# Kernel optimization log

Hardware: AMD Instinct MI355X
Metric: run time of the kernel (lower is better)

## Reference

```python
import jax, jax.numpy as jnp
import numpy as np

FS = 2048
LOWER_FREQ = 16.0
UPPER_FREQ = 512.0
N_SCALES = 64
SIZE_FACTOR = 1.0


def _build_ricker_bank():
    # Geometric scale grid from 1/upper_freq to 1/lower_freq
    s0 = 1.0 / UPPER_FREQ
    sn = 1.0 / LOWER_FREQ
    base = np.power(sn / s0, 1.0 / (N_SCALES - 1))
    scales = s0 * np.power(base, np.arange(N_SCALES))  # [n_scales]
    truncation = scales.max() * np.sqrt(4.5) * FS
    one_side = int(SIZE_FACTOR * truncation)
    kernel_size = 2 * one_side + 1  # 543 for these settings
    k = np.arange(kernel_size, dtype=np.float32) - one_side
    t = k / FS  # [K]
    s = scales[:, None].astype(np.float32)  # [n_scales, 1]
    A = 2.0 / (np.sqrt(3.0 * s) * np.pi ** 0.25)
    scaled_t = t[None, :] / s
    bank = A * (1.0 - scaled_t ** 2) * np.exp(-t[None, :] ** 2 / (2.0 * s ** 2))
    return jnp.asarray(bank, dtype=jnp.float32)  # [n_scales, K]


def setup_inputs() -> dict:
    key = jax.random.key(0)
    inputs = jax.random.normal(key, (128, 4096), dtype=jnp.float32)
    W = _build_ricker_bank()  # [64, 543]
    return {"inputs": inputs, "W": W}


def reference(inputs, W):
    # inputs: [B, T]; W: [n_scales, K] Ricker wavelet bank (real-only).
    # Torch does conv2d on [B,1,T,1] with weight [n_scales,1,K,1], padding K//2
    # (K odd -> 'same' length). border_crop=0, imaginary_part=None, so the
    # scalogram is just the real convolution output.
    K = W.shape[1]
    out = jax.lax.conv_general_dilated(
        inputs[:, None, :],          # [B, 1, T]
        W[:, None, :],               # [n_scales, 1, K]
        window_strides=(1,),
        padding=[(K // 2, K // 2)],
        dimension_numbers=("NCH", "OIH", "NCH"),
    )
    return out  # [B, n_scales, T]
```

## Files before the change

### kernel.cpp

```cpp
#include <hip/hip_runtime.h>


#define TLEN  4096
#define NSC   64
#define KLEN  543
#define KPAD  544
#define PADL  271
#define BLOCK 256
#define TT    512
#define XSRC  1056
#define XLEN  1048
#define XREG  1048
#define NKS   34

typedef __attribute__((ext_vector_type(8)))  short  short8;
typedef __attribute__((ext_vector_type(16))) float  float16v;
typedef __attribute__((ext_vector_type(4)))  float  float4v;

__device__ __forceinline__ ushort f2bf(float f) {
    unsigned u = __builtin_bit_cast(unsigned, f);
    unsigned r = (u + 0x7FFFu + ((u >> 16) & 1u)) >> 16;
    return (ushort)r;
}

__global__ __launch_bounds__(256)
void wconv(const float* __restrict__ W, ushort* __restrict__ wpk)
{
    int idx  = blockIdx.x * 256 + threadIdx.x;
    int e    = idx & 7;
    int lane = (idx >> 3) & 63;
    int st   = (idx >> 9) & 1;
    int ks   = idx >> 10;
    int n    = lane & 31;
    int q5   = lane >> 5;
    int s    = 32 * st + n;
    int k    = 16 * ks + 8 * q5 + e;
    float v  = (k < KLEN) ? W[(size_t)s * KLEN + k] : 0.0f;
    wpk[idx] = f2bf(v);
}

__global__ __launch_bounds__(BLOCK, 2)
void ricker_mfma2(const float* __restrict__ x,
                  const ushort* __restrict__ wpk,
                  float* __restrict__ out)
{
    __shared__ __align__(16) ushort xraw[XSRC];
    __shared__ __align__(16) ushort xsm[8 * XREG];

    const int tid    = threadIdx.x;
    const int tTile  = blockIdx.x;
    const int b      = blockIdx.y;
    const int tStart = tTile * TT;

    const float* xrow = x + (size_t)b * TLEN;
    for (int i = tid; i < XSRC; i += BLOCK) {
        int g = tStart - PADL + i;
        float v = (g >= 0 && g < TLEN) ? xrow[g] : 0.0f;
        xraw[i] = f2bf(v);
    }
    __syncthreads();

    for (int idx = tid; idx < 8 * XLEN; idx += BLOCK) {
        int c = idx / XLEN;
        int i = idx - c * XLEN;
        xsm[c * XREG + i] = xraw[i + c];
    }
    __syncthreads();

    const int lane = tid & 63;
    const int wv   = tid >> 6;
    const int n    = lane & 31;
    const int q5   = lane >> 5;
    const int wt0  = wv * 128;

    const ushort* abase = &xsm[(n & 7) * XREG + 8 * (n >> 3) + 8 * q5 + wt0];
    const ushort* bbase = wpk + (size_t)lane * 8;

    float16v acc[4][2];
    #pragma unroll
    for (int tt = 0; tt < 4; ++tt)
        #pragma unroll
        for (int st = 0; st < 2; ++st)
            #pragma unroll
            for (int e = 0; e < 16; ++e) acc[tt][st][e] = 0.f;

    #pragma unroll 2
    for (int ks = 0; ks < NKS; ++ks) {
        const int K0 = 16 * ks;
        const int BO = 1024 * ks;
        short8 bb0 = *(const short8*)&bbase[BO];
        short8 bb1 = *(const short8*)&bbase[BO + 512];
        short8 a[4];
        #pragma unroll
        for (int tt = 0; tt < 4; ++tt)
            a[tt] = *(const short8*)&abase[K0 + 32 * tt];
        #pragma unroll
        for (int tt = 0; tt < 4; ++tt) {
            acc[tt][0] = __builtin_amdgcn_mfma_f32_32x32x16_bf16(a[tt], bb0, acc[tt][0], 0, 0, 0);
            acc[tt][1] = __builtin_amdgcn_mfma_f32_32x32x16_bf16(a[tt], bb1, acc[tt][1], 0, 0, 0);
        }
    }

    const int tb = tStart + wt0 + 4 * q5;
    float* obase = out + (size_t)b * NSC * TLEN;
    #pragma unroll
    for (int st = 0; st < 2; ++st) {
        #pragma unroll
        for (int tt = 0; tt < 4; ++tt) {
            float16v A = acc[tt][st];
            float* o = obase + (size_t)(32 * st + n) * TLEN + tb + 32 * tt;
            #pragma unroll
            for (int r4 = 0; r4 < 4; ++r4) {
                *(float4v*)&o[8 * r4] =
                    (float4v){A[4 * r4], A[4 * r4 + 1], A[4 * r4 + 2], A[4 * r4 + 3]};
            }
        }
    }
}

extern "C" void kernel_launch(void* const* d_in, const int* in_sizes, int n_in,
                              void* d_out, int out_size, void* d_ws, size_t ws_size,
                              hipStream_t stream) {
    const float* x   = (const float*)d_in[0];
    const float* W   = (const float*)d_in[1];
    float*       out = (float*)d_out;
    ushort*      wpk = (ushort*)d_ws;

    wconv<<<dim3((NSC * KPAD) / 256), dim3(256), 0, stream>>>(W, wpk);
    dim3 grid(TLEN / TT, 128);
    ricker_mfma2<<<grid, dim3(BLOCK), 0, stream>>>(x, wpk, out);
}
```

Measured before the change: 165.1 us.

## Stream weight tiles into LDS with async global_load_lds multi-stage pipeline

Replaces direct per-iteration global loads of the packed weight fragments with a 4-deep per-wave ring buffer filled by global_load_lds, using explicit vmcnt waits so the loads for upcoming k-steps overlap the MFMA work. The MFMA block is wrapped in s_setprio to favour matrix issue. The shifted-copy construction of the input tile is also vectorised to 16-byte short8 reads and writes. This adds 32KB of LDS per block, which may lower occupancy below the two blocks per CU requested in launch bounds. The hand-written waitcnt values also have to match the compiler's emitted loads exactly.

```diff
diff --git a/kernel.cpp b/kernel.cpp
--- a/kernel.cpp
+++ b/kernel.cpp
@@ -46,6 +46,7 @@
 {
     __shared__ __align__(16) ushort xraw[XSRC];
     __shared__ __align__(16) ushort xsm[8 * XREG];
+    __shared__ __align__(16) ushort wsm[4][4][1024];
 
     const int tid    = threadIdx.x;
     const int tTile  = blockIdx.x;
@@ -60,10 +61,21 @@
     }
     __syncthreads();
 
-    for (int idx = tid; idx < 8 * XLEN; idx += BLOCK) {
-        int c = idx / XLEN;
-        int i = idx - c * XLEN;
-        xsm[c * XREG + i] = xraw[i + c];
+    {
+        const short8* xr8 = (const short8*)xraw;
+        short8*       xs8 = (short8*)xsm;
+        for (int j = tid; j < 131; j += BLOCK) {
+            short8 lo = xr8[j];
+            short8 hi = xr8[j + 1];
+            #pragma unroll
+            for (int c = 0; c < 8; ++c) {
+                short8 r;
+                #pragma unroll
+                for (int e = 0; e < 8; ++e)
+                    r[e] = (c + e < 8) ? lo[c + e] : hi[c + e - 8];
+                xs8[c * 131 + j] = r;
+            }
+        }
     }
     __syncthreads();
 
@@ -74,7 +86,7 @@
     const int wt0  = wv * 128;
 
     const ushort* abase = &xsm[(n & 7) * XREG + 8 * (n >> 3) + 8 * q5 + wt0];
-    const ushort* bbase = wpk + (size_t)lane * 8;
+    const ushort* bglob = wpk + (size_t)lane * 8;
 
     float16v acc[4][2];
     #pragma unroll
@@ -84,22 +96,53 @@
             #pragma unroll
             for (int e = 0; e < 16; ++e) acc[tt][st][e] = 0.f;
 
-    #pragma unroll 2
-    for (int ks = 0; ks < NKS; ++ks) {
-        const int K0 = 16 * ks;
-        const int BO = 1024 * ks;
-        short8 bb0 = *(const short8*)&bbase[BO];
-        short8 bb1 = *(const short8*)&bbase[BO + 512];
-        short8 a[4];
-        #pragma unroll
-        for (int tt = 0; tt < 4; ++tt)
-            a[tt] = *(const short8*)&abase[K0 + 32 * tt];
-        #pragma unroll
-        for (int tt = 0; tt < 4; ++tt) {
-            acc[tt][0] = __builtin_amdgcn_mfma_f32_32x32x16_bf16(a[tt], bb0, acc[tt][0], 0, 0, 0);
-            acc[tt][1] = __builtin_amdgcn_mfma_f32_32x32x16_bf16(a[tt], bb1, acc[tt][1], 0, 0, 0);
-        }
+#define STAGE(kss) do {                                                          \
+        const ushort* g0_ = bglob + 1024 * (kss);                                \
+        __builtin_amdgcn_global_load_lds(                                        \
+            (const __attribute__((address_space(1))) void*)g0_,                  \
+            (__attribute__((address_space(3))) void*)&wsm[wv][(kss) & 3][0],     \
+            16, 0, 0);                                                           \
+        __builtin_amdgcn_global_load_lds(                                        \
+            (const __attribute__((address_space(1))) void*)(g0_ + 512),          \
+            (__attribute__((address_space(3))) void*)&wsm[wv][(kss) & 3][512],   \
+            16, 0, 0);                                                           \
+    } while (0)
+
+#define KSTEP(kss, WAITASM) do {                                                 \
+        asm volatile(WAITASM ::: "memory");                                      \
+        __builtin_amdgcn_sched_barrier(0);                                       \
+        const ushort* wrow_ = &wsm[wv][(kss) & 3][0];                            \
+        short8 bb0 = *(const short8*)&wrow_[lane * 8];                           \
+        short8 bb1 = *(const short8*)&wrow_[512 + lane * 8];                     \
+        const int K0_ = 16 * (kss);                                              \
+        short8 a0 = *(const short8*)&abase[K0_];                                 \
+        short8 a1 = *(const short8*)&abase[K0_ + 32];                            \
+        short8 a2 = *(const short8*)&abase[K0_ + 64];                            \
+        short8 a3 = *(const short8*)&abase[K0_ + 96];                            \
+        __builtin_amdgcn_s_setprio(1);                                           \
+        acc[0][0] = __builtin_amdgcn_mfma_f32_32x32x16_bf16(a0, bb0, acc[0][0], 0, 0, 0); \
+        acc[0][1] = __builtin_amdgcn_mfma_f32_32x32x16_bf16(a0, bb1, acc[0][1], 0, 0, 0); \
+        acc[1][0] = __builtin_amdgcn_mfma_f32_32x32x16_bf16(a1, bb0, acc[1][0], 0, 0, 0); \
+        acc[1][1] = __builtin_amdgcn_mfma_f32_32x32x16_bf16(a1, bb1, acc[1][1], 0, 0, 0); \
+        acc[2][0] = __builtin_amdgcn_mfma_f32_32x32x16_bf16(a2, bb0, acc[2][0], 0, 0, 0); \
+        acc[2][1] = __builtin_amdgcn_mfma_f32_32x32x16_bf16(a2, bb1, acc[2][1], 0, 0, 0); \
+        acc[3][0] = __builtin_amdgcn_mfma_f32_32x32x16_bf16(a3, bb0, acc[3][0], 0, 0, 0); \
+        acc[3][1] = __builtin_amdgcn_mfma_f32_32x32x16_bf16(a3, bb1, acc[3][1], 0, 0, 0); \
+        __builtin_amdgcn_s_setprio(0);                                           \
+    } while (0)
+
+    STAGE(0); STAGE(1); STAGE(2);
+
+    for (int ks = 0; ks < NKS - 3; ++ks) {
+        STAGE(ks + 3);
+        KSTEP(ks, "s_waitcnt vmcnt(6)");
     }
+    KSTEP(NKS - 3, "s_waitcnt vmcnt(4)");
+    KSTEP(NKS - 2, "s_waitcnt vmcnt(2)");
+    KSTEP(NKS - 1, "s_waitcnt vmcnt(0)");
+
+#undef STAGE
+#undef KSTEP
 
     const int tb = tStart + wt0 + 4 * q5;
     float* obase = out + (size_t)b * NSC * TLEN;
```

Measured after the change: 171.2 us. 1.04x slower.
